# Performance work log

Measured on AMD Instinct MI355X. Metric: run time of the kernel, lower is better.

## Reference

```python
import jax, jax.numpy as jnp
import numpy as np

N, C_IN, C_OUT, H, W = 64, 128, 128, 64, 64
K, RED = 3, 16


def setup_inputs() -> dict:
    key = jax.random.key(0)
    ks = jax.random.split(key, 12)
    s = 0.02
    return {
        "x": jax.random.normal(ks[0], (N, C_IN, H, W), dtype=jnp.float32),
        # spatial_extractor: Linear(16 -> 9)
        "W_sp": jax.random.normal(ks[1], (16, K * K), dtype=jnp.float32) * s,
        "b_sp": jnp.zeros((K * K,), dtype=jnp.float32),
        # out_channel_extractor: Linear(C_IN -> C_OUT//RED) -> ReLU -> Linear(-> C_OUT)
        "W_o1": jax.random.normal(ks[2], (C_IN, C_OUT // RED), dtype=jnp.float32) * s,
        "b_o1": jnp.zeros((C_OUT // RED,), dtype=jnp.float32),
        "W_o2": jax.random.normal(ks[3], (C_OUT // RED, C_OUT), dtype=jnp.float32) * s,
        "b_o2": jnp.zeros((C_OUT,), dtype=jnp.float32),
        # in_channel_extractor: Linear(C_IN -> C_IN//RED) -> ReLU -> Linear(-> C_IN)
        "W_i1": jax.random.normal(ks[4], (C_IN, C_IN // RED), dtype=jnp.float32) * s,
        "b_i1": jnp.zeros((C_IN // RED,), dtype=jnp.float32),
        "W_i2": jax.random.normal(ks[5], (C_IN // RED, C_IN), dtype=jnp.float32) * s,
        "b_i2": jnp.zeros((C_IN,), dtype=jnp.float32),
    }


def reference(x, W_sp, b_sp, W_o1, b_o1, W_o2, b_o2, W_i1, b_i1, W_i2, b_i2):
    n, c, h, w = x.shape
    # AdaptiveAvgPool2d(4): H,W divisible by 4 -> exact 16x16 mean pooling
    xs = x.reshape(n, c, 4, h // 4, 4, w // 4).mean(axis=(3, 5))  # [n,c,4,4]
    xs = xs.reshape(n, c, 16).mean(axis=1)                        # [n,16]
    sp = (xs @ W_sp + b_sp).reshape(n, K, K)                      # [n,3,3]
    gap = x.mean(axis=(2, 3))                                     # [n,C_in]
    co = jax.nn.relu(gap @ W_o1 + b_o1) @ W_o2 + b_o2             # [n,C_out]
    ci = jax.nn.relu(gap @ W_i1 + b_i1) @ W_i2 + b_i2             # [n,C_in]
    # per-sample kernel: [n, C_out, C_in, K, K]
    weight = (co[:, :, None, None, None] * ci[:, None, :, None, None]
              * sp[:, None, None, :, :])

    def per_sample_conv(xi, wi):
        # xi: [C_in,H,W], wi: [C_out,C_in,K,K]
        return jax.lax.conv_general_dilated(
            xi[None], wi, window_strides=(1, 1),
            padding=[(1, 1), (1, 1)])[0]

    return jax.vmap(per_sample_conv)(x, weight)  # [n,C_out,H,W]
```

## Files before the change

kernel.cpp:

```cpp
#include <hip/hip_runtime.h>

#define NB   64
#define CIN  128
#define COUT 128
#define HH   64
#define WW   64
#define HW   4096

typedef float f4v __attribute__((ext_vector_type(4)));


__global__ __launch_bounds__(256) void k_stats(const float* __restrict__ x,
                                               const float* __restrict__ W_i2,
                                               const float* __restrict__ b_i2,
                                               float* __restrict__ gapp,
                                               float* __restrict__ xsmp,
                                               float* __restrict__ B) {
    const int bid = blockIdx.x;
    const int n  = bid >> 3;
    const int rt = bid & 7;
    const int tid = threadIdx.x;
    const int cs = tid >> 7;
    const int p  = tid & 127;
    const int row = p >> 4;
    const int colq = p & 15;
    const int wv = tid >> 6;
    const int cb = colq >> 2;

    __shared__ float lw[2][9][64];
    __shared__ float bsw[4][4][72];
    __shared__ float cacc[9][4][128];

    for (int k = tid; k < 1152; k += 256) {
        const int half = k / 576, jj = (k % 576) >> 6, c = k & 63;
        lw[half][jj][c] = (jj == 8) ? b_i2[half * 64 + c]
                                    : W_i2[jj * CIN + half * 64 + c];
    }
    __syncthreads();

    float4 acc[9];
    #pragma unroll
    for (int j = 0; j < 9; ++j) acc[j] = make_float4(0.f, 0.f, 0.f, 0.f);

    const size_t xbase = ((size_t)n * CIN + cs * 64) * HW
                       + (size_t)(rt * 8 + row) * WW + colq * 4;
    const bool rep = (tid & 0x33) == 0;

    #pragma unroll 4
    for (int c = 0; c < 64; ++c) {
        f4v v = __builtin_nontemporal_load((const f4v*)(x + xbase + (size_t)c * HW));
        #pragma unroll
        for (int j = 0; j < 9; ++j) {
            const float w = lw[cs][j][c];
            acc[j].x += w * v.x; acc[j].y += w * v.y;
            acc[j].z += w * v.z; acc[j].w += w * v.w;
        }
        float ls = (v.x + v.y) + (v.z + v.w);
        ls += __shfl_xor(ls, 1,  64);
        ls += __shfl_xor(ls, 2,  64);
        ls += __shfl_xor(ls, 16, 64);
        ls += __shfl_xor(ls, 32, 64);
        if (rep) bsw[wv][cb][c] = ls;
    }
    __syncthreads();

    if (cs == 1) {
        #pragma unroll
        for (int j = 0; j < 9; ++j) {
            cacc[j][0][p] = acc[j].x; cacc[j][1][p] = acc[j].y;
            cacc[j][2][p] = acc[j].z; cacc[j][3][p] = acc[j].w;
        }
    }

    if (tid < 128) {
        const int half = tid >> 6, c = tid & 63;
        float s = 0.0f;
        #pragma unroll
        for (int q = 0; q < 4; ++q)
            s += bsw[half * 2][q][c] + bsw[half * 2 + 1][q][c];
        gapp[((size_t)n * 8 + rt) * 128 + half * 64 + c] = s;
    }
    {
        const int colb = wv, c = tid & 63;
        float s2 = bsw[0][colb][c] + bsw[1][colb][c]
                 + bsw[2][colb][c] + bsw[3][colb][c];
        s2 += __shfl_xor(s2, 1,  64);
        s2 += __shfl_xor(s2, 2,  64);
        s2 += __shfl_xor(s2, 4,  64);
        s2 += __shfl_xor(s2, 8,  64);
        s2 += __shfl_xor(s2, 16, 64);
        s2 += __shfl_xor(s2, 32, 64);
        if (c == 0) xsmp[((size_t)n * 8 + rt) * 4 + colb] = s2;
    }
    __syncthreads();

    if (cs == 0) {
        const size_t bpix = (size_t)(rt * 8 + row) * WW + colq * 4;
        #pragma unroll
        for (int j = 0; j < 9; ++j) {
            f4v v;
            v.x = acc[j].x + cacc[j][0][p];
            v.y = acc[j].y + cacc[j][1][p];
            v.z = acc[j].z + cacc[j][2][p];
            v.w = acc[j].w + cacc[j][3][p];
            __builtin_nontemporal_store(v, (f4v*)(B + ((size_t)j * NB + n) * HW + bpix));
        }
    }
}

__global__ __launch_bounds__(256) void k_out(
    const float* __restrict__ B,
    const float* __restrict__ gapp, const float* __restrict__ xsmp,
    const float* __restrict__ W_sp, const float* __restrict__ b_sp,
    const float* __restrict__ W_o1, const float* __restrict__ b_o1,
    const float* __restrict__ W_o2, const float* __restrict__ b_o2,
    const float* __restrict__ W_i1, const float* __restrict__ b_i1,
    float* __restrict__ out)
{
    const int bid = blockIdx.x;
    const int n  = bid >> 3;
    const int y0 = (bid & 7) * 8;
    const int tid = threadIdx.x;

    __shared__ float lgap[128];
    __shared__ float lxsm[16];
    __shared__ float lh[16];
    __shared__ float lco[128];
    __shared__ float lsp[9];
    __shared__ float ts[10][66];

    if (tid < 128) {
        float s = 0.0f;
        #pragma unroll
        for (int rt = 0; rt < 8; ++rt)
            s += gapp[((size_t)n * 8 + rt) * 128 + tid];
        lgap[tid] = s * (1.0f / 4096.0f);
    }
    if (tid < 16) {
        const int rowblk = tid >> 2, colb = tid & 3;
        const float s = xsmp[((size_t)n * 8 + rowblk * 2) * 4 + colb]
                      + xsmp[((size_t)n * 8 + rowblk * 2 + 1) * 4 + colb];
        lxsm[tid] = s * (1.0f / 32768.0f);
    }
    __syncthreads();

    if (tid < 8) {
        float acc = b_o1[tid];
        for (int i = 0; i < 128; ++i) acc += lgap[i] * W_o1[i * 8 + tid];
        lh[tid] = fmaxf(acc, 0.0f);
    } else if (tid < 16) {
        const int j = tid - 8;
        float acc = b_i1[j];
        for (int i = 0; i < 128; ++i) acc += lgap[i] * W_i1[i * 8 + j];
        lh[tid] = fmaxf(acc, 0.0f);
    }
    __syncthreads();

    if (tid < 128) {
        float acco = b_o2[tid];
        #pragma unroll
        for (int j = 0; j < 8; ++j) acco += lh[j] * W_o2[j * 128 + tid];
        lco[tid] = acco;
    }
    if (tid < 9) {
        float acc = b_sp[tid];
        #pragma unroll
        for (int j = 0; j < 16; ++j) acc += lxsm[j] * W_sp[j * 9 + tid];
        lsp[tid] = acc;
    }
    __syncthreads();

    if (tid < 160) {
        const int ry = tid >> 4, cq = tid & 15;
        const int gy = y0 - 1 + ry;
        float4 tv = make_float4(0.f, 0.f, 0.f, 0.f);
        if (gy >= 0 && gy < HH) {
            const size_t pix = (size_t)gy * WW + cq * 4;
            const float* Bn = B + (size_t)n * HW + pix;
            float4 a = *(const float4*)(Bn + (size_t)8 * NB * HW);
            tv = a;
            #pragma unroll
            for (int j = 0; j < 8; ++j) {
                const float h = lh[8 + j];
                float4 u = *(const float4*)(Bn + (size_t)j * NB * HW);
                tv.x += h * u.x; tv.y += h * u.y;
                tv.z += h * u.z; tv.w += h * u.w;
            }
        }
        ts[ry][cq * 4 + 0] = tv.x; ts[ry][cq * 4 + 1] = tv.y;
        ts[ry][cq * 4 + 2] = tv.z; ts[ry][cq * 4 + 3] = tv.w;
    }
    __syncthreads();

    const int i = tid & 127;
    const int row = i >> 4;
    const int cc0 = (i & 15) * 4;
    float sv[4];
    #pragma unroll
    for (int u = 0; u < 4; ++u) {
        const int cc = cc0 + u;
        float acc = 0.0f;
        #pragma unroll
        for (int dy = 0; dy < 3; ++dy) {
            #pragma unroll
            for (int dx = 0; dx < 3; ++dx) {
                const int cx = cc + dx - 1;
                if (cx >= 0 && cx < WW)
                    acc += lsp[dy * 3 + dx] * ts[row + dy][cx];
            }
        }
        sv[u] = acc;
    }

    const int ohalf = (tid >> 7) * 64;
    float* outp = out + (size_t)n * COUT * HW + (size_t)y0 * WW + (size_t)i * 4;
    #pragma unroll 4
    for (int op = 0; op < 64; ++op) {
        const int o = ohalf + op;
        const float scl = lco[o];
        f4v v; v.x = sv[0] * scl; v.y = sv[1] * scl; v.z = sv[2] * scl; v.w = sv[3] * scl;
        __builtin_nontemporal_store(v, (f4v*)(outp + (size_t)o * HW));
    }
}

extern "C" void kernel_launch(void* const* d_in, const int* in_sizes, int n_in,
                              void* d_out, int out_size, void* d_ws, size_t ws_size,
                              hipStream_t stream) {
    const float* x    = (const float*)d_in[0];
    const float* W_sp = (const float*)d_in[1];
    const float* b_sp = (const float*)d_in[2];
    const float* W_o1 = (const float*)d_in[3];
    const float* b_o1 = (const float*)d_in[4];
    const float* W_o2 = (const float*)d_in[5];
    const float* b_o2 = (const float*)d_in[6];
    const float* W_i1 = (const float*)d_in[7];
    const float* b_i1 = (const float*)d_in[8];
    const float* W_i2 = (const float*)d_in[9];
    const float* b_i2 = (const float*)d_in[10];

    float* ws = (float*)d_ws;
    float* gapp = ws;
    float* xsmp = ws + 65536;
    float* B    = ws + 73728;
    float* out  = (float*)d_out;

    k_stats<<<NB * 8, 256, 0, stream>>>(x, W_i2, b_i2, gapp, xsmp, B);
    k_out<<<NB * 8, 256, 0, stream>>>(B, gapp, xsmp, W_sp, b_sp, W_o1, b_o1,
                                      W_o2, b_o2, W_i1, b_i1, out);
}
```

Before: 281.6 us.

## Split per-sample coefficient MLP into separate kernel and streamline stats reductions

```diff
diff --git a/kernel.cpp b/kernel.cpp
--- a/kernel.cpp
+++ b/kernel.cpp
@@ -25,42 +25,60 @@
     const int row = p >> 4;
     const int colq = p & 15;
     const int wv = tid >> 6;
+    const int lane = tid & 63;
     const int cb = colq >> 2;
 
-    __shared__ float lw[2][9][64];
-    __shared__ float bsw[4][4][72];
+    __shared__ __align__(16) float lwt[2][64][12];
+    __shared__ float bsw2[128][33];
     __shared__ float cacc[9][4][128];
+    __shared__ float xw[4][4];
 
     for (int k = tid; k < 1152; k += 256) {
-        const int half = k / 576, jj = (k % 576) >> 6, c = k & 63;
-        lw[half][jj][c] = (jj == 8) ? b_i2[half * 64 + c]
-                                    : W_i2[jj * CIN + half * 64 + c];
+        const int half = k / 576;
+        const int r = k - half * 576;
+        const int c = r / 9;
+        const int j = r - c * 9;
+        lwt[half][c][j] = (j == 8) ? b_i2[half * 64 + c]
+                                   : W_i2[j * CIN + half * 64 + c];
     }
     __syncthreads();
 
     float4 acc[9];
     #pragma unroll
     for (int j = 0; j < 9; ++j) acc[j] = make_float4(0.f, 0.f, 0.f, 0.f);
+    float xacc = 0.0f;
 
     const size_t xbase = ((size_t)n * CIN + cs * 64) * HW
                        + (size_t)(rt * 8 + row) * WW + colq * 4;
-    const bool rep = (tid & 0x33) == 0;
+    const int widx = ((wv & 1) << 4) | ((lane >> 4) << 2) | cb;
+    const bool rep = (lane & 3) == 0;
 
     #pragma unroll 4
     for (int c = 0; c < 64; ++c) {
         f4v v = __builtin_nontemporal_load((const f4v*)(x + xbase + (size_t)c * HW));
+        const float4 wa = *(const float4*)(&lwt[cs][c][0]);
+        const float4 wb = *(const float4*)(&lwt[cs][c][4]);
+        const float w8 = lwt[cs][c][8];
+        const float wjs[9] = {wa.x, wa.y, wa.z, wa.w, wb.x, wb.y, wb.z, wb.w, w8};
         #pragma unroll
         for (int j = 0; j < 9; ++j) {
-            const float w = lw[cs][j][c];
-            acc[j].x += w * v.x; acc[j].y += w * v.y;
-            acc[j].z += w * v.z; acc[j].w += w * v.w;
+            acc[j].x += wjs[j] * v.x; acc[j].y += wjs[j] * v.y;
+            acc[j].z += wjs[j] * v.z; acc[j].w += wjs[j] * v.w;
         }
         float ls = (v.x + v.y) + (v.z + v.w);
-        ls += __shfl_xor(ls, 1,  64);
-        ls += __shfl_xor(ls, 2,  64);
-        ls += __shfl_xor(ls, 16, 64);
-        ls += __shfl_xor(ls, 32, 64);
-        if (rep) bsw[wv][cb][c] = ls;
+        xacc += ls;
+        ls += __shfl_xor(ls, 1, 64);
+        ls += __shfl_xor(ls, 2, 64);
+        if (rep) bsw2[cs * 64 + c][widx] = ls;
+    }
+
+    {
+        float xs2 = xacc;
+        xs2 += __shfl_xor(xs2, 1,  64);
+        xs2 += __shfl_xor(xs2, 2,  64);
+        xs2 += __shfl_xor(xs2, 16, 64);
+        xs2 += __shfl_xor(xs2, 32, 64);
+        if ((lane & 0x33) == 0) xw[wv][cb] = xs2;
     }
     __syncthreads();
 
@@ -73,100 +91,114 @@
     }
 
     if (tid < 128) {
-        const int half = tid >> 6, c = tid & 63;
         float s = 0.0f;
         #pragma unroll
-        for (int q = 0; q < 4; ++q)
-            s += bsw[half * 2][q][c] + bsw[half * 2 + 1][q][c];
-        gapp[((size_t)n * 8 + rt) * 128 + half * 64 + c] = s;
-    }
-    {
-        const int colb = wv, c = tid & 63;
-        float s2 = bsw[0][colb][c] + bsw[1][colb][c]
-                 + bsw[2][colb][c] + bsw[3][colb][c];
-        s2 += __shfl_xor(s2, 1,  64);
-        s2 += __shfl_xor(s2, 2,  64);
-        s2 += __shfl_xor(s2, 4,  64);
-        s2 += __shfl_xor(s2, 8,  64);
-        s2 += __shfl_xor(s2, 16, 64);
-        s2 += __shfl_xor(s2, 32, 64);
-        if (c == 0) xsmp[((size_t)n * 8 + rt) * 4 + colb] = s2;
-    }
-    __syncthreads();
+        for (int k = 0; k < 32; ++k) s += bsw2[tid][k];
+        gapp[((size_t)n * 8 + rt) * 128 + tid] = s;
+    }
+    __syncthreads();
+
+    if (tid < 4) {
+        xsmp[((size_t)n * 8 + rt) * 4 + tid] =
+            xw[0][tid] + xw[1][tid] + xw[2][tid] + xw[3][tid];
+    }
 
     if (cs == 0) {
         const size_t bpix = (size_t)(rt * 8 + row) * WW + colq * 4;
         #pragma unroll
         for (int j = 0; j < 9; ++j) {
-            f4v v;
-            v.x = acc[j].x + cacc[j][0][p];
-            v.y = acc[j].y + cacc[j][1][p];
-            v.z = acc[j].z + cacc[j][2][p];
-            v.w = acc[j].w + cacc[j][3][p];
-            __builtin_nontemporal_store(v, (f4v*)(B + ((size_t)j * NB + n) * HW + bpix));
-        }
-    }
-}
-
-__global__ __launch_bounds__(256) void k_out(
-    const float* __restrict__ B,
+            f4v v2;
+            v2.x = acc[j].x + cacc[j][0][p];
+            v2.y = acc[j].y + cacc[j][1][p];
+            v2.z = acc[j].z + cacc[j][2][p];
+            v2.w = acc[j].w + cacc[j][3][p];
+            __builtin_nontemporal_store(v2, (f4v*)(B + ((size_t)j * NB + n) * HW + bpix));
+        }
+    }
+}
+
+__global__ __launch_bounds__(128) void k_coef(
     const float* __restrict__ gapp, const float* __restrict__ xsmp,
     const float* __restrict__ W_sp, const float* __restrict__ b_sp,
     const float* __restrict__ W_o1, const float* __restrict__ b_o1,
     const float* __restrict__ W_o2, const float* __restrict__ b_o2,
     const float* __restrict__ W_i1, const float* __restrict__ b_i1,
-    float* __restrict__ out)
+    float* __restrict__ coef)
+{
+    const int n = blockIdx.x;
+    const int tid = threadIdx.x;
+    __shared__ float lgap[128];
+    __shared__ float lxsm[16];
+    __shared__ float lh[16];
+
+    {
+        float s = 0.0f;
+        #pragma unroll
+        for (int rtv = 0; rtv < 8; ++rtv)
+            s += gapp[((size_t)n * 8 + rtv) * 128 + tid];
+        lgap[tid] = s * (1.0f / 4096.0f);
+    }
+    if (tid < 16) {
+        const int rb = tid >> 2, cbk = tid & 3;
+        const float s = xsmp[((size_t)n * 8 + rb * 2) * 4 + cbk]
+                      + xsmp[((size_t)n * 8 + rb * 2 + 1) * 4 + cbk];
+        lxsm[tid] = s * (1.0f / 32768.0f);
+    }
+    __syncthreads();
+
+    {
+        const int wvv = tid >> 6, lane = tid & 63;
+        const int j = lane >> 3, ch = lane & 7;
+        const float* Wm = wvv ? W_i1 : W_o1;
+        const float* bm = wvv ? b_i1 : b_o1;
+        float a = 0.0f;
+        #pragma unroll
+        for (int i = 0; i < 16; ++i)
+            a += lgap[ch * 16 + i] * Wm[(ch * 16 + i) * 8 + j];
+        a += __shfl_xor(a, 1, 64);
+        a += __shfl_xor(a, 2, 64);
+        a += __shfl_xor(a, 4, 64);
+        if (ch == 0) lh[wvv * 8 + j] = fmaxf(a + bm[j], 0.0f);
+    }
+    __syncthreads();
+
+    float* cf = coef + (size_t)n * 160;
+    {
+        float acco = b_o2[tid];
+        #pragma unroll
+        for (int jj = 0; jj < 8; ++jj) acco += lh[jj] * W_o2[jj * 128 + tid];
+        cf[tid] = acco;
+    }
+    if (tid < 9) {
+        float a = b_sp[tid];
+        #pragma unroll
+        for (int jj = 0; jj < 16; ++jj) a += lxsm[jj] * W_sp[jj * 9 + tid];
+        cf[128 + tid] = a;
+    }
+    if (tid < 8) cf[137 + tid] = lh[8 + tid];
+}
+
+__global__ __launch_bounds__(256) void k_out(const float* __restrict__ B,
+                                             const float* __restrict__ coef,
+                                             float* __restrict__ out)
 {
     const int bid = blockIdx.x;
     const int n  = bid >> 3;
     const int y0 = (bid & 7) * 8;
     const int tid = threadIdx.x;
 
-    __shared__ float lgap[128];
-    __shared__ float lxsm[16];
-    __shared__ float lh[16];
+    __shared__ float lh[8];
     __shared__ float lco[128];
     __shared__ float lsp[9];
-    __shared__ float ts[10][66];
-
-    if (tid < 128) {
-        float s = 0.0f;
-        #pragma unroll
-        for (int rt = 0; rt < 8; ++rt)
-            s += gapp[((size_t)n * 8 + rt) * 128 + tid];
-        lgap[tid] = s * (1.0f / 4096.0f);
-    }
-    if (tid < 16) {
-        const int rowblk = tid >> 2, colb = tid & 3;
-        const float s = xsmp[((size_t)n * 8 + rowblk * 2) * 4 + colb]
-                      + xsmp[((size_t)n * 8 + rowblk * 2 + 1) * 4 + colb];
-        lxsm[tid] = s * (1.0f / 32768.0f);
-    }
-    __syncthreads();
-
-    if (tid < 8) {
-        float acc = b_o1[tid];
-        for (int i = 0; i < 128; ++i) acc += lgap[i] * W_o1[i * 8 + tid];
-        lh[tid] = fmaxf(acc, 0.0f);
-    } else if (tid < 16) {
-        const int j = tid - 8;
-        float acc = b_i1[j];
-        for (int i = 0; i < 128; ++i) acc += lgap[i] * W_i1[i * 8 + j];
-        lh[tid] = fmaxf(acc, 0.0f);
-    }
-    __syncthreads();
-
-    if (tid < 128) {
-        float acco = b_o2[tid];
-        #pragma unroll
-        for (int j = 0; j < 8; ++j) acco += lh[j] * W_o2[j * 128 + tid];
-        lco[tid] = acco;
-    }
-    if (tid < 9) {
-        float acc = b_sp[tid];
-        #pragma unroll
-        for (int j = 0; j < 16; ++j) acc += lxsm[j] * W_sp[j * 9 + tid];
-        lsp[tid] = acc;
+    __shared__ float ts[10][67];
+
+    const float* cf = coef + (size_t)n * 160;
+    if (tid < 128)       lco[tid]       = cf[tid];
+    else if (tid < 137)  lsp[tid - 128] = cf[tid];
+    else if (tid < 145)  lh[tid - 137]  = cf[tid];
+    if (tid >= 160 && tid < 180) {
+        const int r = (tid - 160) >> 1;
+        ts[r][((tid - 160) & 1) * 65] = 0.0f;
     }
     __syncthreads();
 
@@ -175,20 +207,18 @@
         const int gy = y0 - 1 + ry;
         float4 tv = make_float4(0.f, 0.f, 0.f, 0.f);
         if (gy >= 0 && gy < HH) {
-            const size_t pix = (size_t)gy * WW + cq * 4;
-            const float* Bn = B + (size_t)n * HW + pix;
-            float4 a = *(const float4*)(Bn + (size_t)8 * NB * HW);
-            tv = a;
+            const float* Bn = B + (size_t)n * HW + (size_t)gy * WW + cq * 4;
+            tv = *(const float4*)(Bn + (size_t)8 * NB * HW);
             #pragma unroll
             for (int j = 0; j < 8; ++j) {
-                const float h = lh[8 + j];
+                const float h = lh[j];
                 float4 u = *(const float4*)(Bn + (size_t)j * NB * HW);
                 tv.x += h * u.x; tv.y += h * u.y;
                 tv.z += h * u.z; tv.w += h * u.w;
             }
         }
-        ts[ry][cq * 4 + 0] = tv.x; ts[ry][cq * 4 + 1] = tv.y;
-        ts[ry][cq * 4 + 2] = tv.z; ts[ry][cq * 4 + 3] = tv.w;
+        ts[ry][cq * 4 + 1] = tv.x; ts[ry][cq * 4 + 2] = tv.y;
+        ts[ry][cq * 4 + 3] = tv.z; ts[ry][cq * 4 + 4] = tv.w;
     }
     __syncthreads();
 
@@ -198,18 +228,14 @@
     float sv[4];
     #pragma unroll
     for (int u = 0; u < 4; ++u) {
-        const int cc = cc0 + u;
-        float acc = 0.0f;
+        float a2 = 0.0f;
         #pragma unroll
         for (int dy = 0; dy < 3; ++dy) {
             #pragma unroll
-            for (int dx = 0; dx < 3; ++dx) {
-                const int cx = cc + dx - 1;
-                if (cx >= 0 && cx < WW)
-                    acc += lsp[dy * 3 + dx] * ts[row + dy][cx];
-            }
-        }
-        sv[u] = acc;
+            for (int dx = 0; dx < 3; ++dx)
+                a2 += lsp[dy * 3 + dx] * ts[row + dy][cc0 + u + dx];
+        }
+        sv[u] = a2;
     }
 
     const int ohalf = (tid >> 7) * 64;
@@ -242,9 +268,11 @@
     float* gapp = ws;
     float* xsmp = ws + 65536;
     float* B    = ws + 73728;
+    float* coef = ws + 2433024;
     float* out  = (float*)d_out;
 
     k_stats<<<NB * 8, 256, 0, stream>>>(x, W_i2, b_i2, gapp, xsmp, B);
-    k_out<<<NB * 8, 256, 0, stream>>>(B, gapp, xsmp, W_sp, b_sp, W_o1, b_o1,
-                                      W_o2, b_o2, W_i1, b_i1, out);
-}
+    k_coef<<<NB, 128, 0, stream>>>(gapp, xsmp, W_sp, b_sp, W_o1, b_o1,
+                                   W_o2, b_o2, W_i1, b_i1, coef);
+    k_out<<<NB * 8, 256, 0, stream>>>(B, coef, out);
+}
```

Measured after the change: 271.8 us. 1.04x faster.
